# Kernel optimization log

Hardware: AMD Instinct MI355X
Metric: run time of the kernel (lower is better)

Reference implementation:

```python
import jax, jax.numpy as jnp
import numpy as np

EPS = 1e-3  # jitter to guarantee SPD input

def setup_inputs() -> dict:
    key = jax.random.key(0)
    B, N = 8192, 64
    a = jax.random.normal(key, (B, N, N), dtype=jnp.float32)
    # build batched SPD matrices: x = A A^T / N + eps I
    x = jnp.einsum('bij,bkj->bik', a, a) / N + EPS * jnp.eye(N, dtype=jnp.float32)
    return {"x": x}

def reference(x) -> jnp.ndarray:
    # LogEig: eigendecompose each SPD matrix, take log of eigenvalues,
    # reconstruct: U diag(log s) U^T
    w, v = jnp.linalg.eigh(x)                       # w: [B,N], v: [B,N,N]
    logw = jnp.log(w)
    # (v * logw[..., None, :]) scales columns of v by log-eigenvalues
    out = jnp.einsum('bik,bk,bjk->bij', v, logw, v)
    return out
```

## Files before the change

### kernel.cpp

```cpp
#include <hip/hip_runtime.h>
#include <math.h>

#define NTHR   512
#define SWEEPS 7

__device__ __forceinline__ int ring_next_even(int s) {
    return (s == 0) ? 0 : ((s == 62) ? 63 : s + 2);
}
__device__ __forceinline__ int ring_next_odd(int s) {
    return (s == 1) ? 2 : s - 2;
}
__device__ __forceinline__ int cpos(int c) {
    return (c >> 1) + ((c & 1) << 5);
}

__global__ __launch_bounds__(NTHR, 8)
void logeig_jacobi(const float* __restrict__ x, float* __restrict__ out) {
    __shared__ __align__(16) float A[64 * 64];
    __shared__ __align__(16) float Vt[64 * 64];
    __shared__ __align__(16) float2 prm[32];
    __shared__ float logw[64];

    const int tid = threadIdx.x;
    const int k   = tid & 31;
    const int hw  = tid >> 5;
    const int d   = hw + 1;
    const int q   = (k + d) & 31;
    const bool act = (d < 16) || (k < 16);

    const int ro00 = (2 * k) * 64 + q;

    const int dRp = ring_next_even(2 * k);
    const int dRq = ring_next_odd(2 * k + 1);
    const int dCp = cpos(ring_next_even(2 * q));
    const int dCq = cpos(ring_next_odd(2 * q + 1));
    const int tRp = ring_next_even(2 * q);
    const int tRq = ring_next_odd(2 * q + 1);
    const int tCp = cpos(ring_next_even(2 * k));
    const int tCq = cpos(ring_next_odd(2 * k + 1));

    const int w00 = dRp * 64 + dCp, w01 = dRp * 64 + dCq;
    const int w10 = dRq * 64 + dCp, w11 = dRq * 64 + dCq;
    const int u00 = tRp * 64 + tCp, u01 = tRp * 64 + tCq;
    const int u10 = tRq * 64 + tCp, u11 = tRq * 64 + tCq;
    const int g00 = dRp * 64 + tCp, g01 = dRp * 64 + tCq;
    const int g10 = dRq * 64 + tCp, g11 = dRq * 64 + tCq;

    const int kv  = tid >> 4;
    const int cch = tid & 15;
    const int vdP = ring_next_even(2 * kv);
    const int vdQ = ring_next_odd(2 * kv + 1);

    const size_t base_el = (size_t)blockIdx.x * 4096;

    {
        const float4* x4 = (const float4*)(x + base_el);
        for (int idx4 = tid; idx4 < 1024; idx4 += NTHR) {
            int i = idx4 >> 4, t = idx4 & 15;
            float4 v = x4[idx4];
            *(float2*)&A[i * 64 + 2 * t]      = make_float2(v.x, v.z);
            *(float2*)&A[i * 64 + 32 + 2 * t] = make_float2(v.y, v.w);
            float4 id;
            id.x = (4 * t + 0 == i) ? 1.0f : 0.0f;
            id.y = (4 * t + 1 == i) ? 1.0f : 0.0f;
            id.z = (4 * t + 2 == i) ? 1.0f : 0.0f;
            id.w = (4 * t + 3 == i) ? 1.0f : 0.0f;
            ((float4*)Vt)[idx4] = id;
        }
    }
    __syncthreads();

    for (int sweep = 0; sweep < SWEEPS; ++sweep) {
        for (int r = 0; r < 63; ++r) {
            float app = 0.0f, apq = 0.0f, aqq = 0.0f, tpar = 0.0f;
            if (tid < 32) {
                app = A[(2 * k) * 64 + k];
                apq = A[(2 * k) * 64 + 32 + k];
                aqq = A[(2 * k + 1) * 64 + 32 + k];
                float c = 1.0f, s = 0.0f;
                if (apq != 0.0f) {
                    float tau = (aqq - app) / (2.0f * apq);
                    tpar = copysignf(1.0f, tau) /
                           (fabsf(tau) + sqrtf(1.0f + tau * tau));
                    c = 1.0f / sqrtf(1.0f + tpar * tpar);
                    s = tpar * c;
                }
                prm[k] = make_float2(c, s);
            }

            float m00 = 0.f, m01 = 0.f, m10 = 0.f, m11 = 0.f;
            if (act) {
                m00 = A[ro00];       m01 = A[ro00 + 32];
                m10 = A[ro00 + 64];  m11 = A[ro00 + 96];
            }
            float4 vtop = *(const float4*)&Vt[(2 * kv) * 64 + 4 * cch];
            float4 vbot = *(const float4*)&Vt[(2 * kv + 1) * 64 + 4 * cch];
            __syncthreads();

            float2 pV = prm[kv];

            if (act) {
                float2 pP = prm[k];
                float2 pQ = prm[q];
                float cP = pP.x, sP = pP.y, cQ = pQ.x, sQ = pQ.y;
                float t00 = cP * m00 - sP * m10, t01 = cP * m01 - sP * m11;
                float t10 = sP * m00 + cP * m10, t11 = sP * m01 + cP * m11;
                float n00 = cQ * t00 - sQ * t01, n01 = sQ * t00 + cQ * t01;
                float n10 = cQ * t10 - sQ * t11, n11 = sQ * t10 + cQ * t11;
                A[w00] = n00;  A[w01] = n01;
                A[w10] = n10;  A[w11] = n11;
                A[u00] = n00;  A[u01] = n10;
                A[u10] = n01;  A[u11] = n11;
            }
            if (tid < 32) {
                A[g00] = app - tpar * apq;
                A[g01] = 0.0f;
                A[g10] = 0.0f;
                A[g11] = aqq + tpar * apq;
            }

            {
                float cV = pV.x, sV = pV.y;
                float4 n0, n1;
                n0.x = cV * vtop.x - sV * vbot.x;  n1.x = sV * vtop.x + cV * vbot.x;
                n0.y = cV * vtop.y - sV * vbot.y;  n1.y = sV * vtop.y + cV * vbot.y;
                n0.z = cV * vtop.z - sV * vbot.z;  n1.z = sV * vtop.z + cV * vbot.z;
                n0.w = cV * vtop.w - sV * vbot.w;  n1.w = sV * vtop.w + cV * vbot.w;
                *(float4*)&Vt[vdP * 64 + 4 * cch] = n0;
                *(float4*)&Vt[vdQ * 64 + 4 * cch] = n1;
            }
            __syncthreads();
        }
    }

    if (tid < 64) {
        int p = (tid >> 1) + ((tid & 1) << 5);
        logw[tid] = logf(A[tid * 64 + p]);
    }
    __syncthreads();

    for (int idx4 = tid; idx4 < 1024; idx4 += NTHR) {
        int kk = idx4 >> 4;
        float lw = logw[kk];
        float4 v = ((float4*)Vt)[idx4];
        v.x *= lw; v.y *= lw; v.z *= lw; v.w *= lw;
        ((float4*)A)[idx4] = v;
    }
    __syncthreads();

    float4* out4 = (float4*)(out + base_el);
    for (int idx4 = tid; idx4 < 1024; idx4 += NTHR) {
        int i = idx4 >> 4, j4 = idx4 & 15;
        float4 acc = make_float4(0.0f, 0.0f, 0.0f, 0.0f);
        #pragma unroll 8
        for (int kk = 0; kk < 64; ++kk) {
            float a = A[kk * 64 + i];
            float4 vv = ((float4*)Vt)[kk * 16 + j4];
            acc.x += a * vv.x; acc.y += a * vv.y;
            acc.z += a * vv.z; acc.w += a * vv.w;
        }
        out4[idx4] = acc;
    }
}

extern "C" void kernel_launch(void* const* d_in, const int* in_sizes, int n_in,
                              void* d_out, int out_size, void* d_ws, size_t ws_size,
                              hipStream_t stream) {
    const float* x = (const float*)d_in[0];
    float* o = (float*)d_out;
    int B = in_sizes[0] / 4096;
    logeig_jacobi<<<B, NTHR, 0, stream>>>(x, o);
}
```

Measured before the change: 4.599 ms.

## Precompute next-round Jacobi rotation parameters during current round with double-buffered params

Moves the Givens rotation parameter computation off the critical path. Designated threads compute the next round's (c,s) from the freshly rotated off-diagonal and diagonal values and write them into a double-buffered prm array. This removes the serial 32-thread tau/sqrt/divide step that ran before the first barrier of every round. The cost is extra shared loads, divisions (tpar recomputed as s/c) and intricate ring-index bookkeeping, with some risk to correctness and numerics.

```diff
diff --git a/kernel.cpp b/kernel.cpp
--- a/kernel.cpp
+++ b/kernel.cpp
@@ -10,16 +10,22 @@
 __device__ __forceinline__ int ring_next_odd(int s) {
     return (s == 1) ? 2 : s - 2;
 }
+__device__ __forceinline__ int ring_prev(int s) {
+    if (s == 0) return 0;
+    if (s == 2) return 1;
+    if (!(s & 1)) return s - 2;
+    if (s == 63) return 62;
+    return s + 2;
+}
 __device__ __forceinline__ int cpos(int c) {
     return (c >> 1) + ((c & 1) << 5);
 }
 
 __global__ __launch_bounds__(NTHR, 8)
 void logeig_jacobi(const float* __restrict__ x, float* __restrict__ out) {
-    __shared__ __align__(16) float A[64 * 64];
-    __shared__ __align__(16) float Vt[64 * 64];
-    __shared__ __align__(16) float2 prm[32];
-    __shared__ float logw[64];
+    __shared__ __align__(16) float  A[64 * 64];
+    __shared__ __align__(16) float  Vt[64 * 64];
+    __shared__ __align__(16) float2 prm[2][32];
 
     const int tid = threadIdx.x;
     const int k   = tid & 31;
@@ -45,6 +51,22 @@
     const int u10 = tRq * 64 + tCp, u11 = tRq * 64 + tCq;
     const int g00 = dRp * 64 + tCp, g01 = dRp * 64 + tCq;
     const int g10 = dRq * 64 + tCp, g11 = dRq * 64 + tCq;
+
+    bool stg = false; int sk = 0;
+    if (d == 1 && (k == 0 || k == 30)) { stg = true; sk = (k == 0) ? 0 : 31; }
+    if (d == 2 && k <= 29)             { stg = true; sk = k + 1; }
+    const int sa = ring_prev(2 * sk);
+    const int sb = ring_prev(2 * sk + 1);
+    const bool evenA = !(sa & 1);
+    const bool evenB = !(sb & 1);
+    const int  nsel  = ((sa & 1) << 1) | (sb & 1);
+
+    const int pa0 = (2 * k) * 64 + k;
+    const int pa1 = (2 * k) * 64 + 32 + k;
+    const int pa2 = (2 * k + 1) * 64 + 32 + k;
+    const int qa0 = (2 * q) * 64 + q;
+    const int qa1 = (2 * q) * 64 + 32 + q;
+    const int qa2 = (2 * q + 1) * 64 + 32 + q;
 
     const int kv  = tid >> 4;
     const int cch = tid & 15;
@@ -70,53 +92,78 @@
     }
     __syncthreads();
 
+    if (tid < 32) {
+        float app = A[pa0], apq = A[pa1], aqq = A[pa2];
+        float c = 1.0f, s = 0.0f;
+        if (apq != 0.0f) {
+            float tau = (aqq - app) / (2.0f * apq);
+            float t   = copysignf(1.0f, tau) /
+                        (fabsf(tau) + sqrtf(1.0f + tau * tau));
+            c = 1.0f / sqrtf(1.0f + t * t);
+            s = t * c;
+        }
+        prm[0][k] = make_float2(c, s);
+    }
+
+    int pi = 0;
     for (int sweep = 0; sweep < SWEEPS; ++sweep) {
         for (int r = 0; r < 63; ++r) {
-            float app = 0.0f, apq = 0.0f, aqq = 0.0f, tpar = 0.0f;
-            if (tid < 32) {
-                app = A[(2 * k) * 64 + k];
-                apq = A[(2 * k) * 64 + 32 + k];
-                aqq = A[(2 * k + 1) * 64 + 32 + k];
-                float c = 1.0f, s = 0.0f;
-                if (apq != 0.0f) {
-                    float tau = (aqq - app) / (2.0f * apq);
-                    tpar = copysignf(1.0f, tau) /
-                           (fabsf(tau) + sqrtf(1.0f + tau * tau));
-                    c = 1.0f / sqrtf(1.0f + tpar * tpar);
-                    s = tpar * c;
-                }
-                prm[k] = make_float2(c, s);
-            }
-
             float m00 = 0.f, m01 = 0.f, m10 = 0.f, m11 = 0.f;
             if (act) {
                 m00 = A[ro00];       m01 = A[ro00 + 32];
                 m10 = A[ro00 + 64];  m11 = A[ro00 + 96];
             }
+            float dg0 = 0.f, dg1 = 0.f, dg2 = 0.f;
+            if (tid < 32) { dg0 = A[pa0]; dg1 = A[pa1]; dg2 = A[pa2]; }
+            float sp0 = 0.f, sp1 = 0.f, sp2 = 0.f;
+            float sq0 = 0.f, sq1 = 0.f, sq2 = 0.f;
+            if (stg) {
+                sp0 = A[pa0]; sp1 = A[pa1]; sp2 = A[pa2];
+                sq0 = A[qa0]; sq1 = A[qa1]; sq2 = A[qa2];
+            }
             float4 vtop = *(const float4*)&Vt[(2 * kv) * 64 + 4 * cch];
             float4 vbot = *(const float4*)&Vt[(2 * kv + 1) * 64 + 4 * cch];
             __syncthreads();
 
-            float2 pV = prm[kv];
-
+            const float2 pP = prm[pi][k];
+            const float2 pQ = prm[pi][q];
+            const float2 pV = prm[pi][kv];
+
+            float n00 = 0.f, n01 = 0.f, n10 = 0.f, n11 = 0.f;
             if (act) {
-                float2 pP = prm[k];
-                float2 pQ = prm[q];
                 float cP = pP.x, sP = pP.y, cQ = pQ.x, sQ = pQ.y;
                 float t00 = cP * m00 - sP * m10, t01 = cP * m01 - sP * m11;
                 float t10 = sP * m00 + cP * m10, t11 = sP * m01 + cP * m11;
-                float n00 = cQ * t00 - sQ * t01, n01 = sQ * t00 + cQ * t01;
-                float n10 = cQ * t10 - sQ * t11, n11 = sQ * t10 + cQ * t11;
+                n00 = cQ * t00 - sQ * t01;  n01 = sQ * t00 + cQ * t01;
+                n10 = cQ * t10 - sQ * t11;  n11 = sQ * t10 + cQ * t11;
                 A[w00] = n00;  A[w01] = n01;
                 A[w10] = n10;  A[w11] = n11;
                 A[u00] = n00;  A[u01] = n10;
                 A[u10] = n01;  A[u11] = n11;
             }
             if (tid < 32) {
-                A[g00] = app - tpar * apq;
+                float tpar = pP.y / pP.x;
+                A[g00] = dg0 - tpar * dg1;
                 A[g01] = 0.0f;
                 A[g10] = 0.0f;
-                A[g11] = aqq + tpar * apq;
+                A[g11] = dg2 + tpar * dg1;
+            }
+            if (stg) {
+                float tp = pP.y / pP.x;
+                float tq = pQ.y / pQ.x;
+                float diagA = evenA ? (sp0 - tp * sp1) : (sp2 + tp * sp1);
+                float diagB = evenB ? (sq0 - tq * sq1) : (sq2 + tq * sq1);
+                float napq  = (nsel == 0) ? n00 : (nsel == 1) ? n01
+                            : (nsel == 2) ? n10 : n11;
+                float c = 1.0f, s = 0.0f;
+                if (napq != 0.0f) {
+                    float tau = (diagB - diagA) / (2.0f * napq);
+                    float t   = copysignf(1.0f, tau) /
+                                (fabsf(tau) + sqrtf(1.0f + tau * tau));
+                    c = 1.0f / sqrtf(1.0f + t * t);
+                    s = t * c;
+                }
+                prm[pi ^ 1][sk] = make_float2(c, s);
             }
 
             {
@@ -129,10 +176,12 @@
                 *(float4*)&Vt[vdP * 64 + 4 * cch] = n0;
                 *(float4*)&Vt[vdQ * 64 + 4 * cch] = n1;
             }
+            pi ^= 1;
             __syncthreads();
         }
     }
 
+    float* logw = (float*)prm;
     if (tid < 64) {
         int p = (tid >> 1) + ((tid & 1) << 5);
         logw[tid] = logf(A[tid * 64 + p]);
```

After: 4.721 ms. 2.6% more time.
